# Optimization experiments

Measured on AMD Instinct MI355X. Metric: run time of the kernel, lower is better.

## Reference

```python
import jax, jax.numpy as jnp
import numpy as np

SEQ_LS = [512, 512, 512, 512]
HEADS = 8
DIM_HEAD = 64
DIM = 512
INNER = HEADS * DIM_HEAD  # 512
N = sum(SEQ_LS)           # 2048
B = 4
EPS = 1e-5

# static modality id per token position: [N]
MOD_IDS = jnp.asarray(np.repeat(np.arange(len(SEQ_LS)), SEQ_LS))


def setup_inputs() -> dict:
    key = jax.random.key(0)
    ks = jax.random.split(key, 6)
    x = jax.random.normal(ks[0], (B, N, DIM), dtype=jnp.float32)
    m_labels = jnp.ones((B, len(SEQ_LS)), dtype=jnp.int64 if jax.config.jax_enable_x64 else jnp.int32)
    gamma = jnp.ones((DIM,), dtype=jnp.float32)
    beta = jnp.zeros((DIM,), dtype=jnp.float32)
    w_qkv = jax.random.normal(ks[1], (DIM, 3 * INNER), dtype=jnp.float32) * (DIM ** -0.5)
    w_out = jax.random.normal(ks[2], (INNER, DIM), dtype=jnp.float32) * (INNER ** -0.5)
    b_out = jnp.zeros((DIM,), dtype=jnp.float32)
    return {"x": x, "m_labels": m_labels, "gamma": gamma, "beta": beta,
            "w_qkv": w_qkv, "w_out": w_out, "b_out": b_out}


def _additive_mask(m_labels):
    # present[b, n] = modality of token n is present in sample b
    present = (m_labels[:, MOD_IDS] != 0)                       # [B, N] bool
    pair_ok = present[:, :, None] & present[:, None, :]         # [B, N, N]
    neg_inf = jnp.float32(-jnp.inf)
    return jnp.where(pair_ok, jnp.float32(0.0), neg_inf)        # [B, N, N]


def reference(x, m_labels, gamma, beta, w_qkv, w_out, b_out):
    # LayerNorm(dim)
    mu = jnp.mean(x, axis=-1, keepdims=True)
    var = jnp.mean(jnp.square(x - mu), axis=-1, keepdims=True)
    xn = (x - mu) * jax.lax.rsqrt(var + EPS) * gamma + beta

    # QKV projection (no bias), split heads
    qkv = jnp.einsum('bnd,de->bne', xn, w_qkv)                  # [B, N, 3*INNER]
    q, k, v = jnp.split(qkv, 3, axis=-1)
    def heads(t):
        return t.reshape(B, N, HEADS, DIM_HEAD).transpose(0, 2, 1, 3)  # [B, H, N, Dh]
    q, k, v = heads(q), heads(k), heads(v)

    scale = DIM_HEAD ** -0.5
    dots = jnp.einsum('bhnd,bhmd->bhnm', q, k) * scale          # [B, H, N, N]
    dots = dots + _additive_mask(m_labels)[:, None, :, :]
    attn = jax.nn.softmax(dots, axis=-1)
    out = jnp.einsum('bhnm,bhmd->bhnd', attn, v)                # [B, H, N, Dh]
    out = out.transpose(0, 2, 1, 3).reshape(B, N, INNER)        # [B, N, INNER]
    return jnp.einsum('bni,io->bno', out, w_out) + b_out        # [B, N, DIM]
```

## Files before the change

kernel.cpp:

```cpp
#include <hip/hip_runtime.h>

#define DIMD 512
#define NTOK 2048
#define HEADS 8
#define DH 64

typedef __attribute__((ext_vector_type(4))) float f32x4;
typedef __attribute__((ext_vector_type(8))) __bf16 bf16x8;
typedef __attribute__((ext_vector_type(4))) short s16x4;

#define MFMA16(a, b, c) __builtin_amdgcn_mfma_f32_16x16x32_bf16((a), (b), (c), 0, 0, 0)
#define MFMAK16(a, b, c) __builtin_amdgcn_mfma_f32_16x16x16bf16_1k((a), (b), (c), 0, 0, 0)

__device__ __forceinline__ unsigned short f2bf(float f) {
  unsigned int u = __float_as_uint(f);
  u += 0x7fffu + ((u >> 16) & 1u);
  return (unsigned short)(u >> 16);
}

__device__ __forceinline__ float fexp2(float x) {
  float r;
  asm("v_exp_f32 %0, %1" : "=v"(r) : "v"(x));
  return r;
}

__device__ __forceinline__ unsigned packhi(float b, float a) {
#if __has_builtin(__builtin_amdgcn_perm)
  return __builtin_amdgcn_perm(__float_as_uint(a), __float_as_uint(b), 0x07060302u);
#else
  return (__float_as_uint(b) >> 16) | (__float_as_uint(a) & 0xffff0000u);
#endif
}

__device__ __forceinline__ void gl2lds16(const void* g, void* l) {
  auto gp = reinterpret_cast<__attribute__((address_space(1))) unsigned int*>(
      reinterpret_cast<unsigned long long>(g));
  auto lp = reinterpret_cast<__attribute__((address_space(3))) unsigned int*>(
      reinterpret_cast<unsigned long long>(l));
  __builtin_amdgcn_global_load_lds(gp, lp, 16, 0, 0);
}

__global__ __launch_bounds__(256) void prep_kernel(const float* __restrict__ x,
                                                   const float* __restrict__ gamma,
                                                   const float* __restrict__ beta,
                                                   const float* __restrict__ w_qkv,
                                                   const float* __restrict__ w_out,
                                                   unsigned short* __restrict__ xn,
                                                   unsigned short* __restrict__ wqkvT,
                                                   unsigned short* __restrict__ woutT) {
  __shared__ float t[32][33];
  const int bid = blockIdx.x;
  if (bid < 2048) {
    const int row = bid * 4 + (threadIdx.x >> 6);
    const int lane = threadIdx.x & 63;
    const float4* xr = (const float4*)(x + (size_t)row * DIMD);
    float4 a = xr[lane];
    float4 b = xr[lane + 64];
    float s = a.x + a.y + a.z + a.w + b.x + b.y + b.z + b.w;
    for (int off = 1; off < 64; off <<= 1) s += __shfl_xor(s, off, 64);
    float mu = s * (1.0f / DIMD);
    float d0 = a.x - mu, d1 = a.y - mu, d2 = a.z - mu, d3 = a.w - mu;
    float e0 = b.x - mu, e1 = b.y - mu, e2 = b.z - mu, e3 = b.w - mu;
    float v = d0 * d0 + d1 * d1 + d2 * d2 + d3 * d3 + e0 * e0 + e1 * e1 + e2 * e2 + e3 * e3;
    for (int off = 1; off < 64; off <<= 1) v += __shfl_xor(v, off, 64);
    float rs = rsqrtf(v * (1.0f / DIMD) + 1e-5f);
    const float4* g4 = (const float4*)gamma;
    const float4* be4 = (const float4*)beta;
    float4 ga = g4[lane], gb = g4[lane + 64];
    float4 ba = be4[lane], bb = be4[lane + 64];
    unsigned p0 = (unsigned)f2bf(d0 * rs * ga.x + ba.x) | ((unsigned)f2bf(d1 * rs * ga.y + ba.y) << 16);
    unsigned p1 = (unsigned)f2bf(d2 * rs * ga.z + ba.z) | ((unsigned)f2bf(d3 * rs * ga.w + ba.w) << 16);
    unsigned p2 = (unsigned)f2bf(e0 * rs * gb.x + bb.x) | ((unsigned)f2bf(e1 * rs * gb.y + bb.y) << 16);
    unsigned p3 = (unsigned)f2bf(e2 * rs * gb.z + bb.z) | ((unsigned)f2bf(e3 * rs * gb.w + bb.w) << 16);
    uint2 w0; w0.x = p0; w0.y = p1;
    uint2 w1; w1.x = p2; w1.y = p3;
    *(uint2*)&xn[(size_t)row * DIMD + lane * 4] = w0;
    *(uint2*)&xn[(size_t)row * DIMD + 256 + lane * 4] = w1;
  } else {
    const float* w;
    unsigned short* wt;
    int C, bx, by;
    if (bid < 2816) { w = w_qkv; wt = wqkvT; C = 1536; bx = (bid - 2048) % 48; by = (bid - 2048) / 48; }
    else            { w = w_out; wt = woutT; C = 512;  bx = (bid - 2816) % 16; by = (bid - 2816) / 16; }
    const int R = 512;
    int tx = threadIdx.x & 31, ty = threadIdx.x >> 5;
    int c0 = bx * 32, r0 = by * 32;
    for (int i = 0; i < 4; i++)
      t[ty + 8 * i][tx] = w[(size_t)(r0 + ty + 8 * i) * C + c0 + tx];
    __syncthreads();
    for (int i = 0; i < 4; i++)
      wt[(size_t)(c0 + ty + 8 * i) * R + r0 + tx] = f2bf(t[tx][ty + 8 * i]);
  }
}

__global__ __launch_bounds__(256, 2) void qkv_gemm(const unsigned short* __restrict__ A,
                                                   const unsigned short* __restrict__ Bt,
                                                   unsigned short* __restrict__ qb,
                                                   unsigned short* __restrict__ kb,
                                                   unsigned short* __restrict__ vtb) {
  __shared__ unsigned short As[2][128 * 64];
  __shared__ unsigned short Bs[2][128 * 64];
  const int tid = threadIdx.x;
  const int wave = tid >> 6, lane = tid & 63;
  const int row16 = lane & 15, quad = lane >> 4;
  const int rho = row16 & 7;
  const int m0 = blockIdx.x * 128;
  const int n0 = blockIdx.y * 128;
  const int rw = (wave & 1) * 64, cw = (wave >> 1) * 64;

  const char* Ab = (const char*)A;
  const char* Bb = (const char*)Bt;
#pragma unroll
  for (int i = 0; i < 4; i++) {
    int idx = i * 256 + tid;
    int r = idx >> 3;
    int c = (idx & 7) ^ (r & 7);
    gl2lds16(Ab + ((size_t)(m0 + r) * DIMD) * 2 + c * 16, (char*)As[0] + idx * 16);
    gl2lds16(Bb + ((size_t)(n0 + r) * DIMD) * 2 + c * 16, (char*)Bs[0] + idx * 16);
  }
  __syncthreads();

  f32x4 acc[4][4] = {};
  for (int kt = 0; kt < 8; kt++) {
    const int buf = kt & 1;
    if (kt < 7) {
      const int k0 = (kt + 1) * 64;
#pragma unroll
      for (int i = 0; i < 4; i++) {
        int idx = i * 256 + tid;
        int r = idx >> 3;
        int c = (idx & 7) ^ (r & 7);
        gl2lds16(Ab + ((size_t)(m0 + r) * DIMD + k0) * 2 + c * 16, (char*)As[buf ^ 1] + idx * 16);
        gl2lds16(Bb + ((size_t)(n0 + r) * DIMD + k0) * 2 + c * 16, (char*)Bs[buf ^ 1] + idx * 16);
      }
    }
#pragma unroll
    for (int ks = 0; ks < 2; ks++) {
      bf16x8 av[4], bv[4];
#pragma unroll
      for (int i = 0; i < 4; i++) {
        int Ra = rw + i * 16 + row16;
        int Rb = cw + i * 16 + row16;
        av[i] = *(const bf16x8*)&As[buf][Ra * 64 + (((ks * 4 + quad) ^ rho) * 8)];
        bv[i] = *(const bf16x8*)&Bs[buf][Rb * 64 + (((ks * 4 + quad) ^ rho) * 8)];
      }
#pragma unroll
      for (int i = 0; i < 4; i++)
#pragma unroll
        for (int j = 0; j < 4; j++) acc[i][j] = MFMA16(av[i], bv[j], acc[i][j]);
    }
    __syncthreads();
  }

  unsigned short* Ct = (unsigned short*)As;
#pragma unroll
  for (int i = 0; i < 4; i++)
#pragma unroll
    for (int j = 0; j < 4; j++)
#pragma unroll
      for (int r = 0; r < 4; r++)
        Ct[(rw + i * 16 + quad * 4 + r) * 136 + cw + j * 16 + row16] = f2bf(acc[i][j][r]);
  __syncthreads();

  const int sect = n0 >> 9;
  const int h0 = (n0 & 511) >> 6;
  const int b = m0 >> 11;
  const int nbase = m0 & 2047;
  if (sect < 2) {
    unsigned short* dst = (sect == 0) ? qb : kb;
#pragma unroll
    for (int i = 0; i < 8; i++) {
      int cid = i * 256 + tid;
      int row = cid >> 4, col0 = (cid & 15) * 8;
      int h = h0 + (col0 >> 6), d0 = col0 & 63;
      uint4 val = *(const uint4*)&Ct[row * 136 + col0];
      *(uint4*)&dst[(((size_t)(b * HEADS + h) * NTOK) + nbase + row) * DH + d0] = val;
    }
  } else {
#pragma unroll
    for (int u = 0; u < 4; u++) {
      int uid = u * 256 + tid;
      int col = uid >> 3, rc = (uid & 7) * 16;
      int h = h0 + (col >> 6), d = col & 63;
      unsigned short tmp[16];
#pragma unroll
      for (int j = 0; j < 16; j++) tmp[j] = Ct[(rc + j) * 136 + col];
      size_t base = ((size_t)(b * HEADS + h) * DH + d) * NTOK + nbase + rc;
      *(uint4*)&vtb[base] = *(uint4*)&tmp[0];
      *(uint4*)&vtb[base + 8] = *(uint4*)&tmp[8];
    }
  }
}

__global__ __launch_bounds__(512) void attn_kernel(const unsigned short* __restrict__ qb,
                                                   const unsigned short* __restrict__ kb,
                                                   const unsigned short* __restrict__ vtb,
                                                   const int* __restrict__ mlab,
                                                   unsigned short* __restrict__ ao) {
  __shared__ unsigned short Qs[256 * 64];
  __shared__ unsigned short Ks[2][64 * 64];
  __shared__ unsigned short Vs[2][64 * 64];
  const int tid = threadIdx.x;
  const int wave = tid >> 6, lane = tid & 63;
  const int row16 = lane & 15, quad = lane >> 4;
  const int rho = row16 & 7;
  const int bh = blockIdx.y;
  const int b = bh >> 3, h = bh & 7;
  const int q0 = blockIdx.x * 256;

  const char* qg = (const char*)(qb + ((size_t)bh * NTOK + q0) * DH);
  const char* kgb = (const char*)(kb + (size_t)bh * NTOK * DH);
  const char* vgb = (const char*)(vtb + (size_t)bh * DH * NTOK);
  const int sr = tid >> 3;
  const int sc = (tid & 7) ^ (sr & 7);

#pragma unroll
  for (int i = 0; i < 4; i++)
    gl2lds16(qg + (sr + 64 * i) * 128 + sc * 16, (char*)Qs + tid * 16 + i * 8192);
  gl2lds16(kgb + sr * 128 + sc * 16, (char*)Ks[0] + tid * 16);
  gl2lds16(vgb + (size_t)sr * 4096 + sc * 16, (char*)Vs[0] + tid * 16);
  __syncthreads();

  bf16x8 aq[2][2];
#pragma unroll
  for (int qs = 0; qs < 2; qs++) {
    const int qrow = wave * 32 + qs * 16 + row16;
#pragma unroll
    for (int ki = 0; ki < 2; ki++)
      aq[qs][ki] = *(const bf16x8*)&Qs[qrow * 64 + (((ki * 4 + quad) ^ rho) * 8)];
  }

  f32x4 accT[4][2] = {};
  float lsum[2] = {0.f, 0.f};
  const float cs = 0.125f * 1.44269504088896f;
  const float c0 = mlab[b * 4 + 0] ? -16.f : -100000.f;
  const float c1 = mlab[b * 4 + 1] ? -16.f : -100000.f;
  const float c2 = mlab[b * 4 + 2] ? -16.f : -100000.f;
  const float c3 = mlab[b * 4 + 3] ? -16.f : -100000.f;

  for (int t = 0; t < 32; t++) {
    const int buf = t & 1;
    if (t < 31) {
      gl2lds16(kgb + (size_t)(t + 1) * 8192 + sr * 128 + sc * 16, (char*)Ks[buf ^ 1] + tid * 16);
      gl2lds16(vgb + (size_t)(t + 1) * 128 + (size_t)sr * 4096 + sc * 16, (char*)Vs[buf ^ 1] + tid * 16);
    }
    f32x4 S[2][4];
#pragma unroll
    for (int f = 0; f < 4; f++) {
      const unsigned short* Kr = &Ks[buf][(f * 16 + row16) * 64];
      bf16x8 ak0 = *(const bf16x8*)&Kr[(quad ^ rho) * 8];
      bf16x8 ak1 = *(const bf16x8*)&Kr[((quad + 4) ^ rho) * 8];
#pragma unroll
      for (int qs = 0; qs < 2; qs++) {
        f32x4 z = {};
        z = MFMA16(ak0, aq[qs][0], z);
        z = MFMA16(ak1, aq[qs][1], z);
        S[qs][f] = z;
      }
    }
    const int mi = t >> 3;
    const float c = (mi == 0) ? c0 : (mi == 1) ? c1 : (mi == 2) ? c2 : c3;
    s16x4 pf[2][4];
#pragma unroll
    for (int qs = 0; qs < 2; qs++)
#pragma unroll
      for (int f = 0; f < 4; f++) {
        float p0 = fexp2(fmaf(S[qs][f][0], cs, c));
        float p1 = fexp2(fmaf(S[qs][f][1], cs, c));
        float p2 = fexp2(fmaf(S[qs][f][2], cs, c));
        float p3 = fexp2(fmaf(S[qs][f][3], cs, c));
        lsum[qs] += (p0 + p1) + (p2 + p3);
        uint2 pk;
        pk.x = packhi(p0, p1);
        pk.y = packhi(p2, p3);
        pf[qs][f] = *(s16x4*)&pk;
      }
#pragma unroll
    for (int g = 0; g < 4; g++) {
      const unsigned short* Vr = &Vs[buf][(g * 16 + row16) * 64];
#pragma unroll
      for (int u = 0; u < 4; u++) {
        s16x4 va = *(const s16x4*)&Vr[(((2 * u + (quad >> 1)) ^ rho) * 8) + (quad & 1) * 4];
#pragma unroll
        for (int qs = 0; qs < 2; qs++) accT[g][qs] = MFMAK16(va, pf[qs][u], accT[g][qs]);
      }
    }
    __syncthreads();
  }

#pragma unroll
  for (int qs = 0; qs < 2; qs++) {
    float s = lsum[qs];
    s += __shfl_xor(s, 16, 64);
    s += __shfl_xor(s, 32, 64);
    lsum[qs] = 1.0f / s;
  }
#pragma unroll
  for (int qs = 0; qs < 2; qs++) {
    const int q = q0 + wave * 32 + qs * 16 + row16;
    unsigned short* aor = ao + ((size_t)b * NTOK + q) * DIMD + h * DH;
#pragma unroll
    for (int g = 0; g < 4; g++) {
      *(unsigned*)&aor[g * 16 + quad * 4] = packhi(accT[g][qs][0] * lsum[qs], accT[g][qs][1] * lsum[qs]);
      *(unsigned*)&aor[g * 16 + quad * 4 + 2] = packhi(accT[g][qs][2] * lsum[qs], accT[g][qs][3] * lsum[qs]);
    }
  }
}

__global__ __launch_bounds__(256, 2) void out_gemm(const unsigned short* __restrict__ A,
                                                   const unsigned short* __restrict__ Bt,
                                                   const float* __restrict__ bias,
                                                   float* __restrict__ out) {
  __shared__ unsigned short As[2][128 * 64];
  __shared__ unsigned short Bs[2][64 * 64];
  const int tid = threadIdx.x;
  const int wave = tid >> 6, lane = tid & 63;
  const int row16 = lane & 15, quad = lane >> 4;
  const int rho = row16 & 7;
  const int m0 = blockIdx.x * 128;
  const int n0 = blockIdx.y * 64;
  const int rw = (wave & 1) * 64, cw = (wave >> 1) * 32;

  const char* Ab = (const char*)A;
  const char* Bb = (const char*)Bt;
#pragma unroll
  for (int i = 0; i < 4; i++) {
    int idx = i * 256 + tid;
    int r = idx >> 3;
    int c = (idx & 7) ^ (r & 7);
    gl2lds16(Ab + ((size_t)(m0 + r) * DIMD) * 2 + c * 16, (char*)As[0] + idx * 16);
  }
#pragma unroll
  for (int i = 0; i < 2; i++) {
    int idx = i * 256 + tid;
    int r = idx >> 3;
    int c = (idx & 7) ^ (r & 7);
    gl2lds16(Bb + ((size_t)(n0 + r) * DIMD) * 2 + c * 16, (char*)Bs[0] + idx * 16);
  }
  __syncthreads();

  f32x4 acc[4][2] = {};
  for (int kt = 0; kt < 8; kt++) {
    const int buf = kt & 1;
    if (kt < 7) {
      const int k0 = (kt + 1) * 64;
#pragma unroll
      for (int i = 0; i < 4; i++) {
        int idx = i * 256 + tid;
        int r = idx >> 3;
        int c = (idx & 7) ^ (r & 7);
        gl2lds16(Ab + ((size_t)(m0 + r) * DIMD + k0) * 2 + c * 16, (char*)As[buf ^ 1] + idx * 16);
      }
#pragma unroll
      for (int i = 0; i < 2; i++) {
        int idx = i * 256 + tid;
        int r = idx >> 3;
        int c = (idx & 7) ^ (r & 7);
        gl2lds16(Bb + ((size_t)(n0 + r) * DIMD + k0) * 2 + c * 16, (char*)Bs[buf ^ 1] + idx * 16);
      }
    }
#pragma unroll
    for (int ks = 0; ks < 2; ks++) {
      bf16x8 av[4], bv[2];
#pragma unroll
      for (int i = 0; i < 4; i++)
        av[i] = *(const bf16x8*)&As[buf][(rw + i * 16 + row16) * 64 + (((ks * 4 + quad) ^ rho) * 8)];
#pragma unroll
      for (int j = 0; j < 2; j++)
        bv[j] = *(const bf16x8*)&Bs[buf][(cw + j * 16 + row16) * 64 + (((ks * 4 + quad) ^ rho) * 8)];
#pragma unroll
      for (int i = 0; i < 4; i++)
#pragma unroll
        for (int j = 0; j < 2; j++) acc[i][j] = MFMA16(av[i], bv[j], acc[i][j]);
    }
    __syncthreads();
  }

#pragma unroll
  for (int j = 0; j < 2; j++) {
    const int col = n0 + cw + j * 16 + row16;
    const float bv = bias[col];
#pragma unroll
    for (int i = 0; i < 4; i++)
#pragma unroll
      for (int r = 0; r < 4; r++) {
        const int row = m0 + rw + i * 16 + quad * 4 + r;
        out[(size_t)row * DIMD + col] = acc[i][j][r] + bv;
      }
  }
}

extern "C" void kernel_launch(void* const* d_in, const int* in_sizes, int n_in,
                              void* d_out, int out_size, void* d_ws, size_t ws_size,
                              hipStream_t stream) {
  const float* x = (const float*)d_in[0];
  const int* mlab = (const int*)d_in[1];
  const float* gamma = (const float*)d_in[2];
  const float* beta = (const float*)d_in[3];
  const float* w_qkv = (const float*)d_in[4];
  const float* w_out = (const float*)d_in[5];
  const float* b_out = (const float*)d_in[6];
  float* out = (float*)d_out;

  char* ws = (char*)d_ws;
  unsigned short* xn = (unsigned short*)(ws);
  unsigned short* wqkvT = (unsigned short*)(ws + 8388608);
  unsigned short* woutT = (unsigned short*)(ws + 9961472);
  unsigned short* qbuf = (unsigned short*)(ws + 10485760);
  unsigned short* kbuf = (unsigned short*)(ws + 18874368);
  unsigned short* vtbuf = (unsigned short*)(ws + 27262976);
  unsigned short* aobuf = (unsigned short*)(ws + 35651584);

  prep_kernel<<<3072, 256, 0, stream>>>(x, gamma, beta, w_qkv, w_out, xn, wqkvT, woutT);
  qkv_gemm<<<dim3(64, 12), 256, 0, stream>>>(xn, wqkvT, qbuf, kbuf, vtbuf);
  attn_kernel<<<dim3(8, 32), 512, 0, stream>>>(qbuf, kbuf, vtbuf, mlab, aobuf);
  out_gemm<<<dim3(64, 8), 256, 0, stream>>>(aobuf, woutT, b_out, out);
}
```

Measured before the change: 155.8 us.

## Use 16 waves per attention block with one query tile per wave

Grows the attention block from 512 to 1024 threads, so each wave handles 16 query rows instead of 32. K and V tile loads are split between the two halves of the block. The goal is more waves in flight and fewer registers per wave, to hide latency better. In exchange, K/V LDS reads are no longer reused across two query subtiles, so each loaded K/V fragment feeds half as many MFMAs and LDS read traffic per FLOP doubles.

```diff
diff --git a/kernel.cpp b/kernel.cpp
--- a/kernel.cpp
+++ b/kernel.cpp
@@ -192,11 +192,11 @@
   }
 }
 
-__global__ __launch_bounds__(512) void attn_kernel(const unsigned short* __restrict__ qb,
-                                                   const unsigned short* __restrict__ kb,
-                                                   const unsigned short* __restrict__ vtb,
-                                                   const int* __restrict__ mlab,
-                                                   unsigned short* __restrict__ ao) {
+__global__ __launch_bounds__(1024, 4) void attn_kernel(const unsigned short* __restrict__ qb,
+                                                       const unsigned short* __restrict__ kb,
+                                                       const unsigned short* __restrict__ vtb,
+                                                       const int* __restrict__ mlab,
+                                                       unsigned short* __restrict__ ao) {
   __shared__ unsigned short Qs[256 * 64];
   __shared__ unsigned short Ks[2][64 * 64];
   __shared__ unsigned short Vs[2][64 * 64];
@@ -211,27 +211,35 @@
   const char* qg = (const char*)(qb + ((size_t)bh * NTOK + q0) * DH);
   const char* kgb = (const char*)(kb + (size_t)bh * NTOK * DH);
   const char* vgb = (const char*)(vtb + (size_t)bh * DH * NTOK);
-  const int sr = tid >> 3;
-  const int sc = (tid & 7) ^ (sr & 7);
-
-#pragma unroll
-  for (int i = 0; i < 4; i++)
-    gl2lds16(qg + (sr + 64 * i) * 128 + sc * 16, (char*)Qs + tid * 16 + i * 8192);
-  gl2lds16(kgb + sr * 128 + sc * 16, (char*)Ks[0] + tid * 16);
-  gl2lds16(vgb + (size_t)sr * 4096 + sc * 16, (char*)Vs[0] + tid * 16);
+
+  const int half = tid >> 9;
+  const int stid = tid & 511;
+  const int sr = stid >> 3;
+  const int sc = (stid & 7) ^ (sr & 7);
+
+#pragma unroll
+  for (int i = 0; i < 2; i++) {
+    int idx = i * 1024 + tid;
+    int r = idx >> 3;
+    int c = (idx & 7) ^ (r & 7);
+    gl2lds16(qg + r * 128 + c * 16, (char*)Qs + idx * 16);
+  }
+  if (half == 0)
+    gl2lds16(kgb + sr * 128 + sc * 16, (char*)Ks[0] + stid * 16);
+  else
+    gl2lds16(vgb + (size_t)sr * 4096 + sc * 16, (char*)Vs[0] + stid * 16);
   __syncthreads();
 
-  bf16x8 aq[2][2];
-#pragma unroll
-  for (int qs = 0; qs < 2; qs++) {
-    const int qrow = wave * 32 + qs * 16 + row16;
+  bf16x8 aq[2];
+  {
+    const int qrow = wave * 16 + row16;
 #pragma unroll
     for (int ki = 0; ki < 2; ki++)
-      aq[qs][ki] = *(const bf16x8*)&Qs[qrow * 64 + (((ki * 4 + quad) ^ rho) * 8)];
-  }
-
-  f32x4 accT[4][2] = {};
-  float lsum[2] = {0.f, 0.f};
+      aq[ki] = *(const bf16x8*)&Qs[qrow * 64 + (((ki * 4 + quad) ^ rho) * 8)];
+  }
+
+  f32x4 accT[4] = {};
+  float lsum = 0.f;
   const float cs = 0.125f * 1.44269504088896f;
   const float c0 = mlab[b * 4 + 0] ? -16.f : -100000.f;
   const float c1 = mlab[b * 4 + 1] ? -16.f : -100000.f;
@@ -241,69 +249,59 @@
   for (int t = 0; t < 32; t++) {
     const int buf = t & 1;
     if (t < 31) {
-      gl2lds16(kgb + (size_t)(t + 1) * 8192 + sr * 128 + sc * 16, (char*)Ks[buf ^ 1] + tid * 16);
-      gl2lds16(vgb + (size_t)(t + 1) * 128 + (size_t)sr * 4096 + sc * 16, (char*)Vs[buf ^ 1] + tid * 16);
-    }
-    f32x4 S[2][4];
+      if (half == 0)
+        gl2lds16(kgb + (size_t)(t + 1) * 8192 + sr * 128 + sc * 16, (char*)Ks[buf ^ 1] + stid * 16);
+      else
+        gl2lds16(vgb + (size_t)(t + 1) * 128 + (size_t)sr * 4096 + sc * 16, (char*)Vs[buf ^ 1] + stid * 16);
+    }
+    f32x4 S[4];
 #pragma unroll
     for (int f = 0; f < 4; f++) {
       const unsigned short* Kr = &Ks[buf][(f * 16 + row16) * 64];
       bf16x8 ak0 = *(const bf16x8*)&Kr[(quad ^ rho) * 8];
       bf16x8 ak1 = *(const bf16x8*)&Kr[((quad + 4) ^ rho) * 8];
-#pragma unroll
-      for (int qs = 0; qs < 2; qs++) {
-        f32x4 z = {};
-        z = MFMA16(ak0, aq[qs][0], z);
-        z = MFMA16(ak1, aq[qs][1], z);
-        S[qs][f] = z;
-      }
+      f32x4 z = {};
+      z = MFMA16(ak0, aq[0], z);
+      z = MFMA16(ak1, aq[1], z);
+      S[f] = z;
     }
     const int mi = t >> 3;
     const float c = (mi == 0) ? c0 : (mi == 1) ? c1 : (mi == 2) ? c2 : c3;
-    s16x4 pf[2][4];
-#pragma unroll
-    for (int qs = 0; qs < 2; qs++)
-#pragma unroll
-      for (int f = 0; f < 4; f++) {
-        float p0 = fexp2(fmaf(S[qs][f][0], cs, c));
-        float p1 = fexp2(fmaf(S[qs][f][1], cs, c));
-        float p2 = fexp2(fmaf(S[qs][f][2], cs, c));
-        float p3 = fexp2(fmaf(S[qs][f][3], cs, c));
-        lsum[qs] += (p0 + p1) + (p2 + p3);
-        uint2 pk;
-        pk.x = packhi(p0, p1);
-        pk.y = packhi(p2, p3);
-        pf[qs][f] = *(s16x4*)&pk;
-      }
+    s16x4 pf[4];
+#pragma unroll
+    for (int f = 0; f < 4; f++) {
+      float p0 = fexp2(fmaf(S[f][0], cs, c));
+      float p1 = fexp2(fmaf(S[f][1], cs, c));
+      float p2 = fexp2(fmaf(S[f][2], cs, c));
+      float p3 = fexp2(fmaf(S[f][3], cs, c));
+      lsum += (p0 + p1) + (p2 + p3);
+      uint2 pk;
+      pk.x = packhi(p0, p1);
+      pk.y = packhi(p2, p3);
+      pf[f] = *(s16x4*)&pk;
+    }
 #pragma unroll
     for (int g = 0; g < 4; g++) {
       const unsigned short* Vr = &Vs[buf][(g * 16 + row16) * 64];
 #pragma unroll
       for (int u = 0; u < 4; u++) {
         s16x4 va = *(const s16x4*)&Vr[(((2 * u + (quad >> 1)) ^ rho) * 8) + (quad & 1) * 4];
-#pragma unroll
-        for (int qs = 0; qs < 2; qs++) accT[g][qs] = MFMAK16(va, pf[qs][u], accT[g][qs]);
+        accT[g] = MFMAK16(va, pf[u], accT[g]);
       }
     }
     __syncthreads();
   }
 
-#pragma unroll
-  for (int qs = 0; qs < 2; qs++) {
-    float s = lsum[qs];
-    s += __shfl_xor(s, 16, 64);
-    s += __shfl_xor(s, 32, 64);
-    lsum[qs] = 1.0f / s;
-  }
-#pragma unroll
-  for (int qs = 0; qs < 2; qs++) {
-    const int q = q0 + wave * 32 + qs * 16 + row16;
-    unsigned short* aor = ao + ((size_t)b * NTOK + q) * DIMD + h * DH;
-#pragma unroll
-    for (int g = 0; g < 4; g++) {
-      *(unsigned*)&aor[g * 16 + quad * 4] = packhi(accT[g][qs][0] * lsum[qs], accT[g][qs][1] * lsum[qs]);
-      *(unsigned*)&aor[g * 16 + quad * 4 + 2] = packhi(accT[g][qs][2] * lsum[qs], accT[g][qs][3] * lsum[qs]);
-    }
+  float s = lsum;
+  s += __shfl_xor(s, 16, 64);
+  s += __shfl_xor(s, 32, 64);
+  const float inv = 1.0f / s;
+  const int q = q0 + wave * 16 + row16;
+  unsigned short* aor = ao + ((size_t)b * NTOK + q) * DIMD + h * DH;
+#pragma unroll
+  for (int g = 0; g < 4; g++) {
+    *(unsigned*)&aor[g * 16 + quad * 4] = packhi(accT[g][0] * inv, accT[g][1] * inv);
+    *(unsigned*)&aor[g * 16 + quad * 4 + 2] = packhi(accT[g][2] * inv, accT[g][3] * inv);
   }
 }
 
@@ -413,6 +411,6 @@
 
   prep_kernel<<<3072, 256, 0, stream>>>(x, gamma, beta, w_qkv, w_out, xn, wqkvT, woutT);
   qkv_gemm<<<dim3(64, 12), 256, 0, stream>>>(xn, wqkvT, qbuf, kbuf, vtbuf);
-  attn_kernel<<<dim3(8, 32), 512, 0, stream>>>(qbuf, kbuf, vtbuf, mlab, aobuf);
+  attn_kernel<<<dim3(8, 32), 1024, 0, stream>>>(qbuf, kbuf, vtbuf, mlab, aobuf);
   out_gemm<<<dim3(64, 8), 256, 0, stream>>>(aobuf, woutT, b_out, out);
 }
```

After: 156.8 us. Within noise of the previous version (+0.7%).

## Split attention key tiles across wave pairs and reduce partial outputs in LDS

Applied to the files above, without the earlier changes.

The attention kernel now gives each wave 64 query rows and half of each 64-key tile, instead of 32 query rows over the full tile. Each K fragment is reused across four query groups and each V fragment read is halved per wave, which cuts LDS reads per MFMA. The two key-halves' partial outputs and row sums are combined through shared memory at the end, and launch bounds now request two blocks per CU. The cost is more accumulator registers, a larger unified shared buffer, and an extra reduction pass with a synchronisation.

```diff
diff --git a/kernel.cpp b/kernel.cpp
--- a/kernel.cpp
+++ b/kernel.cpp
@@ -192,23 +192,25 @@
   }
 }
 
-__global__ __launch_bounds__(512) void attn_kernel(const unsigned short* __restrict__ qb,
-                                                   const unsigned short* __restrict__ kb,
-                                                   const unsigned short* __restrict__ vtb,
-                                                   const int* __restrict__ mlab,
-                                                   unsigned short* __restrict__ ao) {
-  __shared__ unsigned short Qs[256 * 64];
-  __shared__ unsigned short Ks[2][64 * 64];
-  __shared__ unsigned short Vs[2][64 * 64];
+__global__ __launch_bounds__(512, 2) void attn_kernel(const unsigned short* __restrict__ qb,
+                                                      const unsigned short* __restrict__ kb,
+                                                      const unsigned short* __restrict__ vtb,
+                                                      const int* __restrict__ mlab,
+                                                      unsigned short* __restrict__ ao) {
+  __shared__ char SMEM[66560];
+  unsigned short* Qs = (unsigned short*)SMEM;
+  unsigned short* KsB = (unsigned short*)(SMEM + 32768);
+  unsigned short* VsB = (unsigned short*)(SMEM + 49152);
   const int tid = threadIdx.x;
   const int wave = tid >> 6, lane = tid & 63;
   const int row16 = lane & 15, quad = lane >> 4;
   const int rho = row16 & 7;
+  const int kw = wave & 1, qw = wave >> 1;
   const int bh = blockIdx.y;
   const int b = bh >> 3, h = bh & 7;
   const int q0 = blockIdx.x * 256;
 
-  const char* qg = (const char*)(qb + ((size_t)bh * NTOK + q0) * DH);
+  const char* qg_ = (const char*)(qb + ((size_t)bh * NTOK + q0) * DH);
   const char* kgb = (const char*)(kb + (size_t)bh * NTOK * DH);
   const char* vgb = (const char*)(vtb + (size_t)bh * DH * NTOK);
   const int sr = tid >> 3;
@@ -216,22 +218,22 @@
 
 #pragma unroll
   for (int i = 0; i < 4; i++)
-    gl2lds16(qg + (sr + 64 * i) * 128 + sc * 16, (char*)Qs + tid * 16 + i * 8192);
-  gl2lds16(kgb + sr * 128 + sc * 16, (char*)Ks[0] + tid * 16);
-  gl2lds16(vgb + (size_t)sr * 4096 + sc * 16, (char*)Vs[0] + tid * 16);
+    gl2lds16(qg_ + (sr + 64 * i) * 128 + sc * 16, SMEM + tid * 16 + i * 8192);
+  gl2lds16(kgb + sr * 128 + sc * 16, (char*)KsB + tid * 16);
+  gl2lds16(vgb + (size_t)sr * 4096 + sc * 16, (char*)VsB + tid * 16);
   __syncthreads();
 
-  bf16x8 aq[2][2];
-#pragma unroll
-  for (int qs = 0; qs < 2; qs++) {
-    const int qrow = wave * 32 + qs * 16 + row16;
+  bf16x8 aq[4][2];
+#pragma unroll
+  for (int g = 0; g < 4; g++) {
+    const int qrow = qw * 64 + g * 16 + row16;
 #pragma unroll
     for (int ki = 0; ki < 2; ki++)
-      aq[qs][ki] = *(const bf16x8*)&Qs[qrow * 64 + (((ki * 4 + quad) ^ rho) * 8)];
-  }
-
-  f32x4 accT[4][2] = {};
-  float lsum[2] = {0.f, 0.f};
+      aq[g][ki] = *(const bf16x8*)&Qs[qrow * 64 + (((ki * 4 + quad) ^ rho) * 8)];
+  }
+
+  f32x4 accT[4][4] = {};
+  float lsum[4] = {0.f, 0.f, 0.f, 0.f};
   const float cs = 0.125f * 1.44269504088896f;
   const float c0 = mlab[b * 4 + 0] ? -16.f : -100000.f;
   const float c1 = mlab[b * 4 + 1] ? -16.f : -100000.f;
@@ -241,68 +243,102 @@
   for (int t = 0; t < 32; t++) {
     const int buf = t & 1;
     if (t < 31) {
-      gl2lds16(kgb + (size_t)(t + 1) * 8192 + sr * 128 + sc * 16, (char*)Ks[buf ^ 1] + tid * 16);
-      gl2lds16(vgb + (size_t)(t + 1) * 128 + (size_t)sr * 4096 + sc * 16, (char*)Vs[buf ^ 1] + tid * 16);
-    }
-    f32x4 S[2][4];
-#pragma unroll
-    for (int f = 0; f < 4; f++) {
-      const unsigned short* Kr = &Ks[buf][(f * 16 + row16) * 64];
+      gl2lds16(kgb + (size_t)(t + 1) * 8192 + sr * 128 + sc * 16,
+               (char*)KsB + (buf ^ 1) * 8192 + tid * 16);
+      gl2lds16(vgb + (size_t)(t + 1) * 128 + (size_t)sr * 4096 + sc * 16,
+               (char*)VsB + (buf ^ 1) * 8192 + tid * 16);
+    }
+    f32x4 S[4][2];
+#pragma unroll
+    for (int f = 0; f < 2; f++) {
+      const unsigned short* Kr = KsB + buf * 4096 + (kw * 32 + f * 16 + row16) * 64;
       bf16x8 ak0 = *(const bf16x8*)&Kr[(quad ^ rho) * 8];
       bf16x8 ak1 = *(const bf16x8*)&Kr[((quad + 4) ^ rho) * 8];
 #pragma unroll
-      for (int qs = 0; qs < 2; qs++) {
+      for (int g = 0; g < 4; g++) {
         f32x4 z = {};
-        z = MFMA16(ak0, aq[qs][0], z);
-        z = MFMA16(ak1, aq[qs][1], z);
-        S[qs][f] = z;
+        z = MFMA16(ak0, aq[g][0], z);
+        z = MFMA16(ak1, aq[g][1], z);
+        S[g][f] = z;
       }
     }
     const int mi = t >> 3;
     const float c = (mi == 0) ? c0 : (mi == 1) ? c1 : (mi == 2) ? c2 : c3;
-    s16x4 pf[2][4];
-#pragma unroll
-    for (int qs = 0; qs < 2; qs++)
-#pragma unroll
-      for (int f = 0; f < 4; f++) {
-        float p0 = fexp2(fmaf(S[qs][f][0], cs, c));
-        float p1 = fexp2(fmaf(S[qs][f][1], cs, c));
-        float p2 = fexp2(fmaf(S[qs][f][2], cs, c));
-        float p3 = fexp2(fmaf(S[qs][f][3], cs, c));
-        lsum[qs] += (p0 + p1) + (p2 + p3);
+    s16x4 pf[4][2];
+#pragma unroll
+    for (int g = 0; g < 4; g++)
+#pragma unroll
+      for (int f = 0; f < 2; f++) {
+        float p0 = fexp2(fmaf(S[g][f][0], cs, c));
+        float p1 = fexp2(fmaf(S[g][f][1], cs, c));
+        float p2 = fexp2(fmaf(S[g][f][2], cs, c));
+        float p3 = fexp2(fmaf(S[g][f][3], cs, c));
+        lsum[g] += (p0 + p1) + (p2 + p3);
         uint2 pk;
         pk.x = packhi(p0, p1);
         pk.y = packhi(p2, p3);
-        pf[qs][f] = *(s16x4*)&pk;
+        pf[g][f] = *(s16x4*)&pk;
       }
 #pragma unroll
     for (int g = 0; g < 4; g++) {
-      const unsigned short* Vr = &Vs[buf][(g * 16 + row16) * 64];
-#pragma unroll
-      for (int u = 0; u < 4; u++) {
-        s16x4 va = *(const s16x4*)&Vr[(((2 * u + (quad >> 1)) ^ rho) * 8) + (quad & 1) * 4];
-#pragma unroll
-        for (int qs = 0; qs < 2; qs++) accT[g][qs] = MFMAK16(va, pf[qs][u], accT[g][qs]);
+      const unsigned short* Vr = VsB + buf * 4096 + (g * 16 + row16) * 64;
+#pragma unroll
+      for (int u = 0; u < 2; u++) {
+        s16x4 va = *(const s16x4*)&Vr[(((kw * 4 + 2 * u + (quad >> 1)) ^ rho) * 8) + (quad & 1) * 4];
+#pragma unroll
+        for (int qg = 0; qg < 4; qg++) accT[g][qg] = MFMAK16(va, pf[qg][u], accT[g][qg]);
       }
     }
     __syncthreads();
   }
 
 #pragma unroll
-  for (int qs = 0; qs < 2; qs++) {
-    float s = lsum[qs];
+  for (int qg = 0; qg < 4; qg++) {
+    float s = lsum[qg];
     s += __shfl_xor(s, 16, 64);
     s += __shfl_xor(s, 32, 64);
-    lsum[qs] = 1.0f / s;
-  }
-#pragma unroll
-  for (int qs = 0; qs < 2; qs++) {
-    const int q = q0 + wave * 32 + qs * 16 + row16;
-    unsigned short* aor = ao + ((size_t)b * NTOK + q) * DIMD + h * DH;
-#pragma unroll
-    for (int g = 0; g < 4; g++) {
-      *(unsigned*)&aor[g * 16 + quad * 4] = packhi(accT[g][qs][0] * lsum[qs], accT[g][qs][1] * lsum[qs]);
-      *(unsigned*)&aor[g * 16 + quad * 4 + 2] = packhi(accT[g][qs][2] * lsum[qs], accT[g][qs][3] * lsum[qs]);
+    lsum[qg] = s;
+  }
+
+  float* Red = (float*)SMEM;
+  float* LRed = (float*)(SMEM + 65536);
+  if (kw) {
+    float* R = Red + qw * 4096;
+#pragma unroll
+    for (int g = 0; g < 4; g++)
+#pragma unroll
+      for (int qg = 0; qg < 4; qg++) {
+        int c2 = (g * 4 + qg) ^ (lane & 15) ^ ((lane & 48) >> 2);
+        *(f32x4*)&R[lane * 64 + c2 * 4] = accT[g][qg];
+      }
+    if (quad == 0)
+#pragma unroll
+      for (int qg = 0; qg < 4; qg++) LRed[qw * 64 + qg * 16 + row16] = lsum[qg];
+  }
+  __syncthreads();
+  if (kw == 0) {
+    float* R = Red + qw * 4096;
+#pragma unroll
+    for (int g = 0; g < 4; g++)
+#pragma unroll
+      for (int qg = 0; qg < 4; qg++) {
+        int c2 = (g * 4 + qg) ^ (lane & 15) ^ ((lane & 48) >> 2);
+        f32x4 o = *(const f32x4*)&R[lane * 64 + c2 * 4];
+        accT[g][qg] += o;
+      }
+    float inv[4];
+#pragma unroll
+    for (int qg = 0; qg < 4; qg++)
+      inv[qg] = 1.0f / (lsum[qg] + LRed[qw * 64 + qg * 16 + row16]);
+#pragma unroll
+    for (int qg = 0; qg < 4; qg++) {
+      const int q = q0 + qw * 64 + qg * 16 + row16;
+      unsigned short* aor = ao + ((size_t)b * NTOK + q) * DIMD + h * DH;
+#pragma unroll
+      for (int g = 0; g < 4; g++) {
+        *(unsigned*)&aor[g * 16 + quad * 4] = packhi(accT[g][qg][0] * inv[qg], accT[g][qg][1] * inv[qg]);
+        *(unsigned*)&aor[g * 16 + quad * 4 + 2] = packhi(accT[g][qg][2] * inv[qg], accT[g][qg][3] * inv[qg]);
+      }
     }
   }
 }
```

Measured after the change: 153.5 us. About the same (-1.5%).
